# Optimization experiments

Measured on AMD Instinct MI355X. Metric: run time of the kernel, lower is better.

The kernel has to match this reference:

```python
import jax, jax.numpy as jnp
import numpy as np
import math

B, T, D, H = 4, 2048, 1024, 16
DH = D // H

def setup_inputs() -> dict:
    key = jax.random.key(0)
    k1, k2, k3, k4, k5 = jax.random.split(key, 5)
    s = 1.0 / math.sqrt(D)
    x = jax.random.normal(k1, (B, T, D), dtype=jnp.float32)
    # causal mask: 1 where attention allowed (j <= i), 0 elsewhere
    mask = jnp.tril(jnp.ones((T, T), dtype=jnp.float32))[None, None, :, :]
    W_qkv = jax.random.normal(k2, (D, 3 * D), dtype=jnp.float32) * s
    b_qkv = jax.random.normal(k3, (3 * D,), dtype=jnp.float32) * 0.02
    W_proj = jax.random.normal(k4, (D, D), dtype=jnp.float32) * s
    b_proj = jax.random.normal(k5, (D,), dtype=jnp.float32) * 0.02
    return {"x": x, "mask": mask, "W_qkv": W_qkv, "b_qkv": b_qkv,
            "W_proj": W_proj, "b_proj": b_proj}

def reference(x, mask, W_qkv, b_qkv, W_proj, b_proj):
    # qkv: [B,T,3D] -> [3,B,H,T,DH]
    qkv = x @ W_qkv + b_qkv
    qkv = qkv.reshape(B, T, 3, H, DH).transpose(2, 0, 3, 1, 4)
    q, k, v = qkv[0], qkv[1], qkv[2]
    scores = jnp.einsum('bhqd,bhkd->bhqk', q, k) / math.sqrt(DH)
    scores = jnp.where(mask == 0, -jnp.inf, scores)
    attn = jax.nn.softmax(scores, axis=-1)  # dropout p=0 -> identity
    out = jnp.einsum('bhqk,bhkd->bhqd', attn, v)
    out = out.transpose(0, 2, 1, 3).reshape(B, T, D)
    return out @ W_proj + b_proj
```

## Files before the change

kernel.cpp:

```cpp
#include <hip/hip_runtime.h>
#include <hip/hip_bf16.h>

typedef __attribute__((ext_vector_type(8))) short short8;
typedef __attribute__((ext_vector_type(4))) float f32x4;
typedef __attribute__((ext_vector_type(16))) float f32x16;
typedef __attribute__((ext_vector_type(4))) unsigned int u32x4;

#define DEV static __device__ __forceinline__

DEV unsigned short bfc(float f) {
    __bf16 h = (__bf16)f;
    return __builtin_bit_cast(unsigned short, h);
}

DEV unsigned int pack2bf(float lo, float hi) {
    return (unsigned int)bfc(lo) | ((unsigned int)bfc(hi) << 16);
}

DEV void gload16(const void* g, void* l) {
    __builtin_amdgcn_global_load_lds(
        (const __attribute__((address_space(1))) unsigned int*)g,
        (__attribute__((address_space(3))) unsigned int*)l, 16, 0, 0);
}

__global__ void cvt_bf16_kernel(const float* __restrict__ in,
                                unsigned short* __restrict__ out, int n4) {
    int stride = gridDim.x * blockDim.x;
    for (int i = blockIdx.x * blockDim.x + threadIdx.x; i < n4; i += stride) {
        float4 v = reinterpret_cast<const float4*>(in)[i];
        ushort4 o;
        o.x = bfc(v.x); o.y = bfc(v.y); o.z = bfc(v.z); o.w = bfc(v.w);
        reinterpret_cast<ushort4*>(out)[i] = o;
    }
}

__global__ void transpose_cvt_kernel(const float* __restrict__ in,
                                     unsigned short* __restrict__ out,
                                     int K, int N) {
    __shared__ float tile[32][33];
    int n0 = blockIdx.x * 32, k0 = blockIdx.y * 32;
    int tx = threadIdx.x & 31, ty = threadIdx.x >> 5;
    #pragma unroll
    for (int i = 0; i < 32; i += 8)
        tile[ty + i][tx] = in[(size_t)(k0 + ty + i) * N + n0 + tx];
    __syncthreads();
    #pragma unroll
    for (int i = 0; i < 32; i += 8)
        out[(size_t)(n0 + ty + i) * K + k0 + tx] = bfc(tile[tx][ty + i]);
}

template <int EPI>
__global__ __launch_bounds__(256) void gemm_bt(
    const unsigned short* __restrict__ A,
    const unsigned short* __restrict__ Bt,
    const float* __restrict__ bias,
    unsigned short* __restrict__ oQ,
    unsigned short* __restrict__ oK,
    unsigned short* __restrict__ oVt,
    float* __restrict__ oP,
    int M, int N, int K) {
    __shared__ unsigned short As[128 * 32];
    __shared__ unsigned short Bs[128 * 32];
    const int tid = threadIdx.x;
    const int wid = tid >> 6, lane = tid & 63;
    const int r = lane & 15, g = lane >> 4;
    const int wm = wid >> 1, wn = wid & 1;
    const int bm = blockIdx.x, bn = blockIdx.y;

    f32x4 acc[4][4];
    #pragma unroll
    for (int i = 0; i < 4; i++)
        #pragma unroll
        for (int j = 0; j < 4; j++) acc[i][j] = (f32x4)(0.f);

    const int nk = K >> 5;
    for (int kt = 0; kt < nk; ++kt) {
        const int k0 = kt << 5;
        __syncthreads();
        #pragma unroll
        for (int it = 0; it < 2; ++it) {
            int c = it * 256 + wid * 64 + lane;
            int row = c >> 2, cc = c & 3;
            int ccs = cc ^ ((row >> 1) & 3);
            gload16(A + (size_t)(bm * 128 + row) * K + k0 + ccs * 8,
                    (char*)As + (it * 256 + wid * 64) * 16);
            gload16(Bt + (size_t)(bn * 128 + row) * K + k0 + ccs * 8,
                    (char*)Bs + (it * 256 + wid * 64) * 16);
        }
        __syncthreads();
        short8 af[4], bfr[4];
        #pragma unroll
        for (int mi = 0; mi < 4; ++mi) {
            int row = wm * 64 + mi * 16 + r;
            af[mi] = *(const short8*)((const char*)As + row * 64 +
                                      ((g ^ ((row >> 1) & 3)) << 4));
        }
        #pragma unroll
        for (int ni = 0; ni < 4; ++ni) {
            int row = wn * 64 + ni * 16 + r;
            bfr[ni] = *(const short8*)((const char*)Bs + row * 64 +
                                       ((g ^ ((row >> 1) & 3)) << 4));
        }
        #pragma unroll
        for (int mi = 0; mi < 4; ++mi)
            #pragma unroll
            for (int ni = 0; ni < 4; ++ni)
                acc[mi][ni] = __builtin_amdgcn_mfma_f32_16x16x32_bf16(
                    af[mi], bfr[ni], acc[mi][ni], 0, 0, 0);
    }

    const float QSCALE = 0.125f;
    #pragma unroll
    for (int ni = 0; ni < 4; ++ni) {
        int n = bn * 128 + wn * 64 + ni * 16 + r;
        float bb = bias[n];
        #pragma unroll
        for (int mi = 0; mi < 4; ++mi) {
            #pragma unroll
            for (int rr = 0; rr < 4; ++rr) {
                int m = bm * 128 + wm * 64 + mi * 16 + g * 4 + rr;
                float v = acc[mi][ni][rr] + bb;
                if (EPI == 0) {
                    int b = m >> 11, t = m & 2047;
                    int s = n >> 10, hh = (n >> 6) & 15, dh = n & 63;
                    size_t bh = (size_t)(b * 16 + hh);
                    if (s == 0)      oQ[(bh * 2048 + t) * 64 + dh] = bfc(v * QSCALE);
                    else if (s == 1) oK[(bh * 2048 + t) * 64 + dh] = bfc(v);
                    else             oVt[(bh * 64 + dh) * 2048 + t] = bfc(v);
                } else {
                    oP[(size_t)m * N + n] = v;
                }
            }
        }
    }
}

__global__ __launch_bounds__(256) void attn_kernel(
    const unsigned short* __restrict__ Q,
    const unsigned short* __restrict__ Kb,
    const unsigned short* __restrict__ Vt,
    unsigned short* __restrict__ O) {
    __shared__ unsigned short Ks[2 * 64 * 64];
    __shared__ unsigned short Vs[2 * 64 * 64];
    const int tid = threadIdx.x, wid = tid >> 6, lane = tid & 63;
    const int ln31 = lane & 31, hi = lane >> 5;

    const int l = blockIdx.y * 16 + blockIdx.x;
    const int u = l & 255, v = l >> 8;
    const int bh = v * 16 + (u >> 4);
    const int qt = (v & 1) ? (15 - (u & 15)) : (u & 15);

    const size_t hoff = (size_t)bh * 2048 * 64;
    const int qrow0 = qt * 128 + wid * 32;
    const int tq = qrow0 + ln31;
    const float NEG_INF = -__builtin_inff();

    short8 qf[4];
    #pragma unroll
    for (int st = 0; st < 4; ++st)
        qf[st] = *(const short8*)(Q + hoff + (size_t)tq * 64 + st * 16 + hi * 8);

    f32x16 oacc[2];
    oacc[0] = (f32x16)(0.f); oacc[1] = (f32x16)(0.f);
    float mrow = NEG_INF, lrow = 0.f;

    auto stage = [&](int buf, int kvb) {
        #pragma unroll
        for (int it = 0; it < 2; ++it) {
            int c = it * 256 + wid * 64 + lane;
            int row = c >> 3, cc = c & 7;
            int ccs = cc ^ (row & 7);
            gload16(Kb + hoff + (size_t)(kvb + row) * 64 + ccs * 8,
                    (char*)Ks + buf * 8192 + (it * 256 + wid * 64) * 16);
            gload16(Vt + hoff + (size_t)row * 2048 + kvb + ccs * 8,
                    (char*)Vs + buf * 8192 + (it * 256 + wid * 64) * 16);
        }
    };

    const int nkv = 2 * qt + 2;
    stage(0, 0);
    for (int kv = 0; kv < nkv; ++kv) {
        const int kvb = kv * 64;
        const int cur = kv & 1;
        __syncthreads();
        if (kv + 1 < nkv) stage(cur ^ 1, kvb + 64);

        if (kvb <= qrow0) {
            const char* Kbase = (const char*)Ks + cur * 8192;
            const char* Vbase = (const char*)Vs + cur * 8192;
            f32x16 s0 = (f32x16)(0.f), s1 = (f32x16)(0.f);
            __builtin_amdgcn_s_setprio(1);
            #pragma unroll
            for (int st = 0; st < 4; ++st) {
                int row0 = ln31, row1 = 32 + ln31;
                short8 kf0 = *(const short8*)(Kbase + row0 * 128 +
                                              (((2 * st + hi) ^ (row0 & 7)) << 4));
                short8 kf1 = *(const short8*)(Kbase + row1 * 128 +
                                              (((2 * st + hi) ^ (row1 & 7)) << 4));
                s0 = __builtin_amdgcn_mfma_f32_32x32x16_bf16(kf0, qf[st], s0, 0, 0, 0);
                s1 = __builtin_amdgcn_mfma_f32_32x32x16_bf16(kf1, qf[st], s1, 0, 0, 0);
            }
            __builtin_amdgcn_s_setprio(0);

            short8 vf[4][2];
            #pragma unroll
            for (int m = 0; m < 4; ++m)
                #pragma unroll
                for (int d = 0; d < 2; ++d) {
                    int row = d * 32 + ln31;
                    vf[m][d] = *(const short8*)(Vbase + row * 128 +
                                                (((2 * m + hi) ^ (row & 7)) << 4));
                }

            if (kvb + 63 > qrow0) {
                const int lim = tq - kvb;
                #pragma unroll
                for (int j = 0; j < 16; ++j) {
                    int krel = (j & 3) + 8 * (j >> 2) + 4 * hi;
                    if (krel > lim)      s0[j] = NEG_INF;
                    if (krel + 32 > lim) s1[j] = NEG_INF;
                }
            }
            float mloc = NEG_INF;
            #pragma unroll
            for (int j = 0; j < 16; ++j)
                mloc = fmaxf(mloc, fmaxf(s0[j], s1[j]));
            mloc = fmaxf(mloc, __shfl_xor(mloc, 32));
            float mnew = fmaxf(mrow, mloc);
            float alpha = __expf(mrow - mnew);
            mrow = mnew;
            float ls = 0.f;
            #pragma unroll
            for (int j = 0; j < 16; ++j) {
                float p0 = __expf(s0[j] - mnew);
                float p1 = __expf(s1[j] - mnew);
                s0[j] = p0; s1[j] = p1;
                ls += p0 + p1;
            }
            ls += __shfl_xor(ls, 32);
            lrow = lrow * alpha + ls;
            #pragma unroll
            for (int j = 0; j < 16; ++j) { oacc[0][j] *= alpha; oacc[1][j] *= alpha; }

            __builtin_amdgcn_s_setprio(1);
            #pragma unroll
            for (int m = 0; m < 4; ++m) {
                const int h = m & 1;
                float pa0, pa1, pb0, pb1, pc0, pc1, pd0, pd1;
                if (m < 2) {
                    pa0 = s0[8*h+0]; pa1 = s0[8*h+1]; pc0 = s0[8*h+2]; pc1 = s0[8*h+3];
                    pb0 = s0[8*h+4]; pb1 = s0[8*h+5]; pd0 = s0[8*h+6]; pd1 = s0[8*h+7];
                } else {
                    pa0 = s1[8*h+0]; pa1 = s1[8*h+1]; pc0 = s1[8*h+2]; pc1 = s1[8*h+3];
                    pb0 = s1[8*h+4]; pb1 = s1[8*h+5]; pd0 = s1[8*h+6]; pd1 = s1[8*h+7];
                }
                unsigned int pkA = pack2bf(pa0, pa1), pkC = pack2bf(pc0, pc1);
                unsigned int pkB = pack2bf(pb0, pb1), pkD = pack2bf(pd0, pd1);
                unsigned int oA = __shfl_xor(pkA, 32), oB = __shfl_xor(pkB, 32);
                unsigned int oC = __shfl_xor(pkC, 32), oD = __shfl_xor(pkD, 32);
                u32x4 w;
                w.x = hi ? oB : pkA;
                w.y = hi ? oD : pkC;
                w.z = hi ? pkB : oA;
                w.w = hi ? pkD : oC;
                short8 pfrag = __builtin_bit_cast(short8, w);
                #pragma unroll
                for (int d = 0; d < 2; ++d)
                    oacc[d] = __builtin_amdgcn_mfma_f32_32x32x16_bf16(vf[m][d], pfrag, oacc[d], 0, 0, 0);
            }
            __builtin_amdgcn_s_setprio(0);
        }
    }

    const int b = bh >> 4, h = bh & 15;
    const float rinv = 1.0f / lrow;
    unsigned short* orow = O + (size_t)(b * 2048 + tq) * 1024 + h * 64;
    #pragma unroll
    for (int d = 0; d < 2; ++d)
        #pragma unroll
        for (int u2 = 0; u2 < 4; ++u2) {
            int dh0 = d * 32 + u2 * 8 + 4 * hi;
            uint2 w;
            w.x = pack2bf(oacc[d][4*u2+0] * rinv, oacc[d][4*u2+1] * rinv);
            w.y = pack2bf(oacc[d][4*u2+2] * rinv, oacc[d][4*u2+3] * rinv);
            *(uint2*)(orow + dh0) = w;
        }
}

extern "C" void kernel_launch(void* const* d_in, const int* in_sizes, int n_in,
                              void* d_out, int out_size, void* d_ws, size_t ws_size,
                              hipStream_t stream) {
    const float* x     = (const float*)d_in[0];
    const float* Wqkv  = (const float*)d_in[2];
    const float* bqkv  = (const float*)d_in[3];
    const float* Wproj = (const float*)d_in[4];
    const float* bproj = (const float*)d_in[5];
    float* out = (float*)d_out;

    char* ws = (char*)d_ws;
    unsigned short* xb  = (unsigned short*)(ws);
    unsigned short* Ob  = (unsigned short*)(ws);
    unsigned short* WqT = (unsigned short*)(ws + (16u << 20));
    unsigned short* WpT = (unsigned short*)(ws + (22u << 20));
    unsigned short* Qb  = (unsigned short*)(ws + (24u << 20));
    unsigned short* Kb  = (unsigned short*)(ws + (40u << 20));
    unsigned short* Vt  = (unsigned short*)(ws + (56u << 20));

    cvt_bf16_kernel<<<2048, 256, 0, stream>>>(x, xb, (8192 * 1024) / 4);
    transpose_cvt_kernel<<<dim3(96, 32), 256, 0, stream>>>(Wqkv, WqT, 1024, 3072);
    transpose_cvt_kernel<<<dim3(32, 32), 256, 0, stream>>>(Wproj, WpT, 1024, 1024);
    gemm_bt<0><<<dim3(64, 24), 256, 0, stream>>>(xb, WqT, bqkv, Qb, Kb, Vt, nullptr,
                                                 8192, 3072, 1024);
    attn_kernel<<<dim3(16, 64), 256, 0, stream>>>(Qb, Kb, Vt, Ob);
    gemm_bt<1><<<dim3(64, 8), 256, 0, stream>>>(Ob, WpT, bproj, nullptr, nullptr,
                                                nullptr, out, 8192, 1024, 1024);
}
```

Measured before the change: 234.0 us.

## Use 256-row query tiles with 8 waves, exp2 softmax, and lazy rescaling

The attention block grows to 512 threads covering 256 query rows, so each staged K/V tile is shared by twice as many waves and total K/V traffic drops. The Q scale now folds in log2(e) so softmax can use exp2f, and the running-output rescale is skipped when no row max in the wave increases. The max and sum reductions are split into independent chains for more instruction-level parallelism. In exchange, the grid has half as many blocks, which may hurt load balance across CUs, and the larger block needs occupancy support under launch_bounds(512,4).

```diff
diff --git a/kernel.cpp b/kernel.cpp
--- a/kernel.cpp
+++ b/kernel.cpp
@@ -109,7 +109,7 @@
                     af[mi], bfr[ni], acc[mi][ni], 0, 0, 0);
     }
 
-    const float QSCALE = 0.125f;
+    const float QSCALE = 0.18033688011112042f;
     #pragma unroll
     for (int ni = 0; ni < 4; ++ni) {
         int n = bn * 128 + wn * 64 + ni * 16 + r;
@@ -135,7 +135,7 @@
     }
 }
 
-__global__ __launch_bounds__(256) void attn_kernel(
+__global__ __launch_bounds__(512, 4) void attn_kernel(
     const unsigned short* __restrict__ Q,
     const unsigned short* __restrict__ Kb,
     const unsigned short* __restrict__ Vt,
@@ -145,13 +145,13 @@
     const int tid = threadIdx.x, wid = tid >> 6, lane = tid & 63;
     const int ln31 = lane & 31, hi = lane >> 5;
 
-    const int l = blockIdx.y * 16 + blockIdx.x;
+    const int l = blockIdx.y * 8 + blockIdx.x;
     const int u = l & 255, v = l >> 8;
-    const int bh = v * 16 + (u >> 4);
-    const int qt = (v & 1) ? (15 - (u & 15)) : (u & 15);
+    const int bh = v * 32 + (u >> 3);
+    const int qt = v ? (7 - (u & 7)) : (u & 7);
 
     const size_t hoff = (size_t)bh * 2048 * 64;
-    const int qrow0 = qt * 128 + wid * 32;
+    const int qrow0 = qt * 256 + wid * 32;
     const int tq = qrow0 + ln31;
     const float NEG_INF = -__builtin_inff();
 
@@ -164,20 +164,20 @@
     oacc[0] = (f32x16)(0.f); oacc[1] = (f32x16)(0.f);
     float mrow = NEG_INF, lrow = 0.f;
 
+    const unsigned short* Kh = Kb + hoff;
+    const unsigned short* Vh = Vt + hoff;
+
     auto stage = [&](int buf, int kvb) {
-        #pragma unroll
-        for (int it = 0; it < 2; ++it) {
-            int c = it * 256 + wid * 64 + lane;
-            int row = c >> 3, cc = c & 7;
-            int ccs = cc ^ (row & 7);
-            gload16(Kb + hoff + (size_t)(kvb + row) * 64 + ccs * 8,
-                    (char*)Ks + buf * 8192 + (it * 256 + wid * 64) * 16);
-            gload16(Vt + hoff + (size_t)row * 2048 + kvb + ccs * 8,
-                    (char*)Vs + buf * 8192 + (it * 256 + wid * 64) * 16);
-        }
+        int c = tid;
+        int row = c >> 3, cc = c & 7;
+        int ccs = cc ^ (row & 7);
+        gload16(Kh + (size_t)(kvb + row) * 64 + ccs * 8,
+                (char*)Ks + buf * 8192 + c * 16);
+        gload16(Vh + (size_t)row * 2048 + kvb + ccs * 8,
+                (char*)Vs + buf * 8192 + c * 16);
     };
 
-    const int nkv = 2 * qt + 2;
+    const int nkv = 4 * qt + 4;
     stage(0, 0);
     for (int kv = 0; kv < nkv; ++kv) {
         const int kvb = kv * 64;
@@ -221,26 +221,36 @@
                     if (krel + 32 > lim) s1[j] = NEG_INF;
                 }
             }
-            float mloc = NEG_INF;
-            #pragma unroll
-            for (int j = 0; j < 16; ++j)
-                mloc = fmaxf(mloc, fmaxf(s0[j], s1[j]));
+            float ma = fmaxf(s0[0], s0[1]), mb = fmaxf(s0[2], s0[3]);
+            float mc = fmaxf(s1[0], s1[1]), md = fmaxf(s1[2], s1[3]);
+            #pragma unroll
+            for (int j = 4; j < 16; j += 4) {
+                ma = fmaxf(ma, fmaxf(s0[j], s0[j+1]));
+                mb = fmaxf(mb, fmaxf(s0[j+2], s0[j+3]));
+                mc = fmaxf(mc, fmaxf(s1[j], s1[j+1]));
+                md = fmaxf(md, fmaxf(s1[j+2], s1[j+3]));
+            }
+            float mloc = fmaxf(fmaxf(ma, mb), fmaxf(mc, md));
             mloc = fmaxf(mloc, __shfl_xor(mloc, 32));
             float mnew = fmaxf(mrow, mloc);
-            float alpha = __expf(mrow - mnew);
+            if (!__all(mloc <= mrow)) {
+                float alpha = exp2f(mrow - mnew);
+                lrow *= alpha;
+                #pragma unroll
+                for (int j = 0; j < 16; ++j) { oacc[0][j] *= alpha; oacc[1][j] *= alpha; }
+            }
             mrow = mnew;
-            float ls = 0.f;
-            #pragma unroll
-            for (int j = 0; j < 16; ++j) {
-                float p0 = __expf(s0[j] - mnew);
-                float p1 = __expf(s1[j] - mnew);
-                s0[j] = p0; s1[j] = p1;
-                ls += p0 + p1;
-            }
+            float la = 0.f, lb = 0.f, lc = 0.f, ld = 0.f;
+            #pragma unroll
+            for (int j = 0; j < 16; j += 2) {
+                float p00 = exp2f(s0[j] - mnew), p01 = exp2f(s0[j+1] - mnew);
+                float p10 = exp2f(s1[j] - mnew), p11 = exp2f(s1[j+1] - mnew);
+                s0[j] = p00; s0[j+1] = p01; s1[j] = p10; s1[j+1] = p11;
+                la += p00; lb += p01; lc += p10; ld += p11;
+            }
+            float ls = (la + lb) + (lc + ld);
             ls += __shfl_xor(ls, 32);
-            lrow = lrow * alpha + ls;
-            #pragma unroll
-            for (int j = 0; j < 16; ++j) { oacc[0][j] *= alpha; oacc[1][j] *= alpha; }
+            lrow += ls;
 
             __builtin_amdgcn_s_setprio(1);
             #pragma unroll
@@ -311,7 +321,7 @@
     transpose_cvt_kernel<<<dim3(32, 32), 256, 0, stream>>>(Wproj, WpT, 1024, 1024);
     gemm_bt<0><<<dim3(64, 24), 256, 0, stream>>>(xb, WqT, bqkv, Qb, Kb, Vt, nullptr,
                                                  8192, 3072, 1024);
-    attn_kernel<<<dim3(16, 64), 256, 0, stream>>>(Qb, Kb, Vt, Ob);
+    attn_kernel<<<dim3(8, 64), 512, 0, stream>>>(Qb, Kb, Vt, Ob);
     gemm_bt<1><<<dim3(64, 8), 256, 0, stream>>>(Ob, WpT, bproj, nullptr, nullptr,
                                                 nullptr, out, 8192, 1024, 1024);
 }
```

New measurement: 277.1 us. 1.18x slower.
